# Kernel tuning notes

Measured on AMD Instinct MI355X. Metric: run time of the kernel, lower is better.

Reference implementation:

```python
import jax, jax.numpy as jnp
import numpy as np
import math

H = 1024      # d_model
NHALF = 32    # d_state // 2
B = 4
L = 4096
DT_MIN, DT_MAX = 1e-3, 1e-1


def setup_inputs() -> dict:
    key = jax.random.key(0)
    k_x, k_dt, k_c, k_d = jax.random.split(key, 4)
    x = jax.random.normal(k_x, (B, L, H), dtype=jnp.float32)
    # log-uniform dt in [dt_min, dt_max]
    log_dt = (jax.random.uniform(k_dt, (H,), dtype=jnp.float32)
              * (math.log(DT_MAX) - math.log(DT_MIN)) + math.log(DT_MIN))
    log_A_real = jnp.log(0.5 * jnp.ones((H, NHALF), dtype=jnp.float32))
    A_imag = math.pi * jnp.broadcast_to(jnp.arange(NHALF, dtype=jnp.float32), (H, NHALF))
    C = jax.random.normal(k_c, (H, NHALF, 2), dtype=jnp.float32) / math.sqrt(NHALF)
    D = jax.random.normal(k_d, (H,), dtype=jnp.float32)
    return {"x": x, "log_dt": log_dt, "log_A_real": log_A_real,
            "A_imag": A_imag, "C": C, "D": D}


def _kernel(log_dt, log_A_real, A_imag, C, L_len):
    """SSM convolution kernel, shape [H, L]."""
    dt = jnp.exp(log_dt)                                   # [H]
    A = -jnp.exp(log_A_real) + 1j * A_imag                 # [H, N/2] complex
    Cc = C[..., 0] + 1j * C[..., 1]                        # [H, N/2]
    dtA = A * dt[:, None]                                  # [H, N/2]
    Cw = Cc * (jnp.exp(dtA) - 1.0) / A                     # [H, N/2]
    l = jnp.arange(L_len)                                  # [L]
    vand = jnp.exp(dtA[..., None] * l)                     # [H, N/2, L] complex
    K = 2.0 * jnp.einsum('hn,hnl->hl', Cw, vand).real      # [H, L]
    return K


def reference(x, log_dt, log_A_real, A_imag, C, D):
    # transposed=False: x is [B, L, H] -> work in [B, H, L]
    xt = jnp.swapaxes(x, -1, -2)                           # [B, H, L]
    Lc = xt.shape[-1]
    K = _kernel(log_dt, log_A_real, A_imag, C, Lc)         # [H, L]
    n = 2 * Lc
    Kf = jnp.fft.rfft(K.astype(jnp.float32), n=n)          # [H, n//2+1]
    xf = jnp.fft.rfft(xt.astype(jnp.float32), n=n)         # [B, H, n//2+1]
    y = jnp.fft.irfft(xf * Kf, n=n)[..., :Lc]              # [B, H, L]
    y = y + xt * D[:, None]
    return jnp.swapaxes(y, -1, -2).astype(x.dtype)         # [B, L, H]
```

## Files before the change

kernel.cpp:

```cpp
#include <hip/hip_runtime.h>
#include <math.h>

#define Lc 4096
#define Hc 1024
#define Bc 4
#define NNc 32

typedef __attribute__((ext_vector_type(8))) short s8v;
typedef __attribute__((ext_vector_type(4))) float f4v;

#define SWB(r, e) ((((r) << 6) + (e)) ^ (((r) & 7) << 3))

__device__ inline unsigned short bf16_rne(float x) {
    unsigned u = __float_as_uint(x);
    unsigned r = (u + 0x7FFFu + ((u >> 16) & 1u)) >> 16;
    return (unsigned short)r;
}

__global__ __launch_bounds__(256) void split_transpose(const float* __restrict__ src,
                                                       unsigned short* __restrict__ dst) {
    __shared__ float tile[64][65];
    int b  = blockIdx.z;
    int h0 = blockIdx.x * 64;
    int l0 = blockIdx.y * 64;
    const float* s = src + (size_t)b * Lc * Hc;
    int tid = threadIdx.x;
#pragma unroll
    for (int it = 0; it < 4; it++) {
        int idx = tid + 256 * it;
        int r = idx >> 4, c4 = idx & 15;
        float4 v = *(const float4*)(s + (size_t)(l0 + r) * Hc + (h0 + 4 * c4));
        tile[r][4 * c4 + 0] = v.x;
        tile[r][4 * c4 + 1] = v.y;
        tile[r][4 * c4 + 2] = v.z;
        tile[r][4 * c4 + 3] = v.w;
    }
    __syncthreads();
#pragma unroll
    for (int it = 0; it < 8; it++) {
        int hh = it * 8 + (tid >> 5);
        int p  = tid & 31;
        float v0 = tile[2 * p + 0][hh];
        float v1 = tile[2 * p + 1][hh];
        unsigned hi = (unsigned)bf16_rne(v0) | ((unsigned)bf16_rne(v1) << 16);
        unsigned short* base = dst + (size_t)(b * Hc + h0 + hh) * 4096;
        *(unsigned*)(base + (l0 + 2 * p)) = hi;
    }
}

__global__ __launch_bounds__(256) void untranspose_bf16(const unsigned short* __restrict__ src,
                                                        float* __restrict__ dst) {
    __shared__ float tile[64][65];
    int b  = blockIdx.z;
    int h0 = blockIdx.x * 64;
    int l0 = blockIdx.y * 64;
    const unsigned short* s = src + (size_t)b * Hc * Lc;
    float* d = dst + (size_t)b * Lc * Hc;
    int tid = threadIdx.x;
#pragma unroll
    for (int it = 0; it < 8; it++) {
        int idx = tid + 256 * it;
        int hh = idx >> 5, dp = idx & 31;
        unsigned v = *(const unsigned*)(s + (size_t)(h0 + hh) * Lc + (l0 + 2 * dp));
        tile[hh][2 * dp]     = __uint_as_float((v & 0xffffu) << 16);
        tile[hh][2 * dp + 1] = __uint_as_float((v >> 16) << 16);
    }
    __syncthreads();
#pragma unroll
    for (int it = 0; it < 4; it++) {
        int idx = tid + 256 * it;
        int r = idx >> 4, c4 = idx & 15;
        f4v v;
        v.x = tile[4 * c4 + 0][r];
        v.y = tile[4 * c4 + 1][r];
        v.z = tile[4 * c4 + 2][r];
        v.w = tile[4 * c4 + 3][r];
        __builtin_nontemporal_store(v, (f4v*)(d + (size_t)(l0 + r) * Hc + (h0 + 4 * c4)));
    }
}

#define MFMA(a, b, c) __builtin_amdgcn_mfma_f32_16x16x32_bf16((a), (b), (c), 0, 0, 0)

__global__ __launch_bounds__(256, 4) void s4d_mfma9(
    const unsigned short* __restrict__ xpl,
    unsigned short* __restrict__ ypl,
    const float* __restrict__ log_dt,
    const float* __restrict__ log_A_real,
    const float* __restrict__ A_imag,
    const float* __restrict__ Cmat,
    const float* __restrict__ Dvec)
{
    __shared__ __align__(16) unsigned short WtH[4096];
    __shared__ __align__(16) unsigned short WpH[4096];
    __shared__ __align__(16) unsigned short TtH[4096];
    __shared__ __align__(16) unsigned short Elds[64 * 72];
    __shared__ float WV[256];
    __shared__ float Ktap[64];
    __shared__ float cAr[NNc], cAi[NNc], c2R[NNc], c2I[NNc], cWSr[NNc], cWSi[NNc];

    const int tid = threadIdx.x;
    const int h   = blockIdx.x;
    const int w   = tid >> 6;
    const int l   = tid & 63;
    const int l15 = l & 15;
    const int grp = l >> 4;
    const int rowoff = (16 * w + l15) * 64;

    s8v xh0, xh1;
    {
        const unsigned short* xb = xpl + (size_t)h * 4096;
        xh0 = *(const s8v*)(xb + rowoff + 8 * grp);
        xh1 = *(const s8v*)(xb + rowoff + 32 + 8 * grp);
    }

    if (tid < NNc) {
        int n = tid;
        float dtv = expf(log_dt[h]);
        float Ar = -expf(log_A_real[h * NNc + n]);
        float Ai = A_imag[h * NNc + n];
        float ar = Ar * dtv, ai = Ai * dtv;
        cAr[n] = ar; cAi[n] = ai;
        float er = expf(ar), sn, cs;
        sincosf(ai, &sn, &cs);
        float numr = er * cs - 1.f, numi = er * sn;
        float inv = 1.f / (Ar * Ar + Ai * Ai);
        float fr = (numr * Ar + numi * Ai) * inv;
        float fi = (numi * Ar - numr * Ai) * inv;
        float Ccr = Cmat[(h * NNc + n) * 2 + 0];
        float Cci = Cmat[(h * NNc + n) * 2 + 1];
        c2R[n] = 2.f * (Ccr * fr - Cci * fi);
        c2I[n] = 2.f * (Ccr * fi + Cci * fr);
        float e64 = expf(64.f * ar), s64, c64;
        sincosf(64.f * ai, &s64, &c64);
        cWSr[n] = e64 * c64; cWSi[n] = e64 * s64;
    }
    __syncthreads();

    {
        int p = tid >> 2, q = tid & 3;
        float acc = 0.f;
#pragma unroll
        for (int i = 0; i < 8; i++) {
            int n = 8 * q + i;
            float fp = (float)p;
            float e = __expf(cAr[n] * fp);
            float sn = __sinf(cAi[n] * fp), cs = __cosf(cAi[n] * fp);
            acc += e * (c2R[n] * cs - c2I[n] * sn);
        }
        WV[p * 4 + q] = acc;
    }
#pragma unroll
    for (int m = 0; m < 2; m++) {
        int u = tid + 256 * m;
        int r = u >> 3, jc = u & 7;
        {
            int n = r & 31, im = r >> 5;
            s8v hv;
#pragma unroll
            for (int i = 0; i < 8; i++) {
                float p = (float)(63 - (jc * 8 + i));
                float e = __expf(cAr[n] * p);
                float sn = __sinf(cAi[n] * p), cs = __cosf(cAi[n] * p);
                hv[i] = (short)bf16_rne(e * (im ? sn : cs));
            }
            *(s8v*)&WtH[SWB(r, jc * 8)] = hv;
        }
        {
            float p = (float)(r + 1);
            s8v hv;
#pragma unroll
            for (int i = 0; i < 8; i++) {
                int c = jc * 8 + i;
                int n = c >> 1;
                float e = __expf(cAr[n] * p);
                float sn = __sinf(cAi[n] * p), cs = __cosf(cAi[n] * p);
                hv[i] = (short)bf16_rne(e * ((c & 1) ? -sn : cs));
            }
            *(s8v*)&WpH[SWB(r, jc * 8)] = hv;
        }
    }
    __syncthreads();

    if (tid < 64) {
        float k = WV[tid * 4] + WV[tid * 4 + 1] + WV[tid * 4 + 2] + WV[tid * 4 + 3];
        if (tid == 0) k += Dvec[h];
        Ktap[tid] = k;
    }
    __syncthreads();

#pragma unroll
    for (int m = 0; m < 2; m++) {
        int u = tid + 256 * m;
        int r = u >> 3, jc = u & 7;
        s8v hv;
#pragma unroll
        for (int i = 0; i < 8; i++) {
            int j = jc * 8 + i;
            hv[i] = (short)bf16_rne((j <= r) ? Ktap[r - j] : 0.f);
        }
        *(s8v*)&TtH[SWB(r, jc * 8)] = hv;
    }

    float qR[2], qI[2], q4R[2], q4I[2], qgR[2], qgI[2], q16R[2], q16I[2], cwR[2], cwI[2];
#pragma unroll
    for (int md = 0; md < 2; md++) {
        int n = md * 16 + l15;
        float qr = cWSr[n], qi = cWSi[n];
        float q2r = fmaf(qr, qr, -(qi * qi)),    q2i = 2.f * qr * qi;
        float q4r = fmaf(q2r, q2r, -(q2i * q2i)), q4i = 2.f * q2r * q2i;
        float q8r = fmaf(q4r, q4r, -(q4i * q4i)), q8i = 2.f * q4r * q4i;
        float q16r = fmaf(q8r, q8r, -(q8i * q8i)), q16i = 2.f * q8r * q8i;
        float q12r = fmaf(q8r, q4r, -(q8i * q4i)), q12i = fmaf(q8r, q4i, q8i * q4r);
        qR[md] = qr; qI[md] = qi;
        q4R[md] = q4r; q4I[md] = q4i;
        qgR[md] = (grp == 0) ? 1.f : (grp == 1) ? q4r : (grp == 2) ? q8r : q12r;
        qgI[md] = (grp == 0) ? 0.f : (grp == 1) ? q4i : (grp == 2) ? q8i : q12i;
        q16R[md] = q16r; q16I[md] = q16i;
        cwR[md] = c2R[n]; cwI[md] = c2I[n];
    }
    __syncthreads();

#pragma unroll
    for (int b = 0; b < Bc; b++) {
        s8v nh0, nh1;
        if (b < Bc - 1) {
            const unsigned short* xb = xpl + (size_t)((b + 1) * Hc + h) * 4096;
            nh0 = *(const s8v*)(xb + rowoff + 8 * grp);
            nh1 = *(const s8v*)(xb + rowoff + 32 + 8 * grp);
        }

        f4v acc[4];
#pragma unroll
        for (int tj = 0; tj < 4; tj++) {
            int row = tj * 16 + l15;
            s8v bh0 = *(const s8v*)&WtH[SWB(row, 8 * grp)];
            s8v bh1 = *(const s8v*)&WtH[SWB(row, 32 + 8 * grp)];
            f4v a = {0.f, 0.f, 0.f, 0.f};
            a = MFMA(xh0, bh0, a);
            a = MFMA(xh1, bh1, a);
            acc[tj] = a;
        }

        float exr[2][4], exi[2][4], gcr[2], gci[2];
#pragma unroll
        for (int md = 0; md < 2; md++) {
            float qr = qR[md], qi = qI[md];
            float e1r = acc[md][0],                       e1i = acc[md + 2][0];
            float e2r = fmaf(qr, e1r, fmaf(-qi, e1i, acc[md][1]));
            float e2i = fmaf(qr, e1i, fmaf( qi, e1r, acc[md + 2][1]));
            float e3r = fmaf(qr, e2r, fmaf(-qi, e2i, acc[md][2]));
            float e3i = fmaf(qr, e2i, fmaf( qi, e2r, acc[md + 2][2]));
            float tr  = fmaf(qr, e3r, fmaf(-qi, e3i, acc[md][3]));
            float ti  = fmaf(qr, e3i, fmaf( qi, e3r, acc[md + 2][3]));
            exr[md][0] = 0.f; exi[md][0] = 0.f;
            exr[md][1] = e1r; exi[md][1] = e1i;
            exr[md][2] = e2r; exi[md][2] = e2i;
            exr[md][3] = e3r; exi[md][3] = e3i;
            float t1r = __shfl_up(tr, 16u, 64), t1i = __shfl_up(ti, 16u, 64);
            float t2r = __shfl_up(tr, 32u, 64), t2i = __shfl_up(ti, 32u, 64);
            float t3r = __shfl_up(tr, 48u, 64), t3i = __shfl_up(ti, 48u, 64);
            if (grp < 1) { t1r = 0.f; t1i = 0.f; }
            if (grp < 2) { t2r = 0.f; t2i = 0.f; }
            if (grp < 3) { t3r = 0.f; t3i = 0.f; }
            float q4r = q4R[md], q4i = q4I[md];
            float q8r = fmaf(q4r, q4r, -(q4i * q4i)), q8i = 2.f * q4r * q4i;
            float gr = t1r, gi = t1i;
            gr = fmaf(q4r, t2r, fmaf(-q4i, t2i, gr));
            gi = fmaf(q4r, t2i, fmaf( q4i, t2r, gi));
            gr = fmaf(q8r, t3r, fmaf(-q8i, t3i, gr));
            gi = fmaf(q8r, t3i, fmaf( q8i, t3r, gi));
            gcr[md] = gr; gci[md] = gi;
            float wvr = fmaf(q4r, gr, fmaf(-q4i, gi, tr));
            float wvi = fmaf(q4r, gi, fmaf( q4i, gr, ti));
            if (l >= 48) {
                int n = md * 16 + l15;
                WV[w * 64 + 2 * n]     = wvr;
                WV[w * 64 + 2 * n + 1] = wvi;
            }
        }
        __syncthreads();

#pragma unroll
        for (int md = 0; md < 2; md++) {
            int n = md * 16 + l15;
            float wcr = 0.f, wci = 0.f;
            if (w >= 1) {
                wcr = WV[(w - 1) * 64 + 2 * n];
                wci = WV[(w - 1) * 64 + 2 * n + 1];
            }
            if (w >= 2) {
                float vr = WV[(w - 2) * 64 + 2 * n], vi = WV[(w - 2) * 64 + 2 * n + 1];
                wcr = fmaf(q16R[md], vr, fmaf(-q16I[md], vi, wcr));
                wci = fmaf(q16R[md], vi, fmaf( q16I[md], vr, wci));
            }
            if (w >= 3) {
                float q32r = fmaf(q16R[md], q16R[md], -(q16I[md] * q16I[md]));
                float q32i = 2.f * q16R[md] * q16I[md];
                float vr = WV[(w - 3) * 64 + 2 * n], vi = WV[(w - 3) * 64 + 2 * n + 1];
                wcr = fmaf(q32r, vr, fmaf(-q32i, vi, wcr));
                wci = fmaf(q32r, vi, fmaf( q32i, vr, wci));
            }
            float cir = fmaf(qgR[md], wcr, fmaf(-qgI[md], wci, gcr[md]));
            float cii = fmaf(qgR[md], wci, fmaf( qgI[md], wcr, gci[md]));
            float qr = qR[md], qi = qI[md];
            float q2r = fmaf(qr, qr, -(qi * qi)),  q2i = 2.f * qr * qi;
            float q3r = fmaf(q2r, qr, -(q2i * qi)), q3i = fmaf(q2r, qi, q2i * qr);
            float pr[4] = {1.f, qr, q2r, q3r};
            float pi[4] = {0.f, qi, q2i, q3i};
#pragma unroll
            for (int r2 = 0; r2 < 4; r2++) {
                float Gr2 = fmaf(pr[r2], cir, fmaf(-pi[r2], cii, exr[md][r2]));
                float Gi2 = fmaf(pr[r2], cii, fmaf( pi[r2], cir, exi[md][r2]));
                float Er2 = fmaf(cwR[md], Gr2, -(cwI[md] * Gi2));
                float Ei2 = fmaf(cwR[md], Gi2,  (cwI[md] * Gr2));
                unsigned pk = (unsigned)bf16_rne(Er2) | ((unsigned)bf16_rne(Ei2) << 16);
                int chunk = 16 * w + 4 * grp + r2;
                *(unsigned*)&Elds[chunk * 72 + 2 * n] = pk;
            }
        }
        __syncthreads();

        s8v ee0 = *(const s8v*)&Elds[(16 * w + l15) * 72 + 8 * grp];
        s8v ee1 = *(const s8v*)&Elds[(16 * w + l15) * 72 + 32 + 8 * grp];
        unsigned short* yp = ypl + (size_t)(b * Hc + h) * 4096;
#pragma unroll
        for (int tj = 0; tj < 4; tj++) {
            int row = tj * 16 + l15;
            int i0 = SWB(row, 8 * grp);
            int i1 = SWB(row, 32 + 8 * grp);
            s8v th0 = *(const s8v*)&TtH[i0];
            s8v th1 = *(const s8v*)&TtH[i1];
            s8v ph0 = *(const s8v*)&WpH[i0];
            s8v ph1 = *(const s8v*)&WpH[i1];
            f4v a = {0.f, 0.f, 0.f, 0.f};
            a = MFMA(xh0, th0, a);
            a = MFMA(xh1, th1, a);
            a = MFMA(ee0, ph0, a);
            a = MFMA(ee1, ph1, a);
#pragma unroll
            for (int r2 = 0; r2 < 4; r2++) {
                int chunk = 16 * w + 4 * grp + r2;
                yp[chunk * 64 + row] = bf16_rne(a[r2]);
            }
        }

        if (b < Bc - 1) { xh0 = nh0; xh1 = nh1; }
    }
}

extern "C" void kernel_launch(void* const* d_in, const int* in_sizes, int n_in,
                              void* d_out, int out_size, void* d_ws, size_t ws_size,
                              hipStream_t stream) {
    const float* x          = (const float*)d_in[0];
    const float* log_dt     = (const float*)d_in[1];
    const float* log_A_real = (const float*)d_in[2];
    const float* A_imag     = (const float*)d_in[3];
    const float* Cmat       = (const float*)d_in[4];
    const float* Dvec       = (const float*)d_in[5];
    float* out = (float*)d_out;

    const size_t plane = (size_t)Bc * Hc * Lc;
    const size_t need  = plane * sizeof(unsigned short);
    if (ws_size < need) return;

    unsigned short* xpl = (unsigned short*)d_ws;

    split_transpose<<<dim3(Hc / 64, Lc / 64, Bc), 256, 0, stream>>>(x, xpl);
    s4d_mfma9<<<Hc, 256, 0, stream>>>(xpl, xpl, log_dt, log_A_real, A_imag, Cmat, Dvec);
    untranspose_bf16<<<dim3(Hc / 64, Lc / 64, Bc), 256, 0, stream>>>(xpl, out);
}
```

Baseline: 62.44 us.

## Hold Toeplitz tap fragments in registers, swap MFMA operands, pack output stores

The per-channel Toeplitz tap matrix is now built directly into register fragments instead of an LDS tile, which removes the TtH buffer and its reads inside the batch loop. The output MFMAs take their operands in swapped order, so each lane's four accumulator values are contiguous along L and go out as one packed 8-byte store instead of four scattered 2-byte stores. WV is double-buffered by batch parity, and the barrier after the Elds writes is dropped because each wave only reads back the chunks it wrote itself. Powers of q are recomputed on the fly instead of being held across the loop, trading extra ALU work and the register-held tap fragments for lower register pressure elsewhere.

```diff
diff --git a/kernel.cpp b/kernel.cpp
--- a/kernel.cpp
+++ b/kernel.cpp
@@ -8,6 +8,7 @@
 
 typedef __attribute__((ext_vector_type(8))) short s8v;
 typedef __attribute__((ext_vector_type(4))) float f4v;
+typedef __attribute__((ext_vector_type(2))) unsigned int u2v;
 
 #define SWB(r, e) ((((r) << 6) + (e)) ^ (((r) & 7) << 3))
 
@@ -81,7 +82,7 @@
 
 #define MFMA(a, b, c) __builtin_amdgcn_mfma_f32_16x16x32_bf16((a), (b), (c), 0, 0, 0)
 
-__global__ __launch_bounds__(256, 4) void s4d_mfma9(
+__global__ __launch_bounds__(256, 4) void s4d_mfma10(
     const unsigned short* __restrict__ xpl,
     unsigned short* __restrict__ ypl,
     const float* __restrict__ log_dt,
@@ -92,9 +93,8 @@
 {
     __shared__ __align__(16) unsigned short WtH[4096];
     __shared__ __align__(16) unsigned short WpH[4096];
-    __shared__ __align__(16) unsigned short TtH[4096];
     __shared__ __align__(16) unsigned short Elds[64 * 72];
-    __shared__ float WV[256];
+    __shared__ float WV[512];
     __shared__ float Ktap[64];
     __shared__ float cAr[NNc], cAi[NNc], c2R[NNc], c2I[NNc], cWSr[NNc], cWSi[NNc];
 
@@ -188,34 +188,34 @@
     }
     __syncthreads();
 
-#pragma unroll
-    for (int m = 0; m < 2; m++) {
-        int u = tid + 256 * m;
-        int r = u >> 3, jc = u & 7;
-        s8v hv;
-#pragma unroll
-        for (int i = 0; i < 8; i++) {
-            int j = jc * 8 + i;
-            hv[i] = (short)bf16_rne((j <= r) ? Ktap[r - j] : 0.f);
-        }
-        *(s8v*)&TtH[SWB(r, jc * 8)] = hv;
-    }
-
-    float qR[2], qI[2], q4R[2], q4I[2], qgR[2], qgI[2], q16R[2], q16I[2], cwR[2], cwI[2];
+    s8v tf[4][2];
+#pragma unroll
+    for (int tj = 0; tj < 4; tj++) {
+        int row = tj * 16 + l15;
+#pragma unroll
+        for (int hf = 0; hf < 2; hf++) {
+            int kb = 32 * hf + 8 * grp;
+            s8v v;
+#pragma unroll
+            for (int i = 0; i < 8; i++) {
+                int idx = row - kb - i;
+                int ic = idx < 0 ? 0 : idx;
+                float kv = Ktap[ic];
+                v[i] = (short)bf16_rne(idx < 0 ? 0.f : kv);
+            }
+            tf[tj][hf] = v;
+        }
+    }
+
+    float qR[2], qI[2], q4R[2], q4I[2], cwR[2], cwI[2];
 #pragma unroll
     for (int md = 0; md < 2; md++) {
         int n = md * 16 + l15;
         float qr = cWSr[n], qi = cWSi[n];
-        float q2r = fmaf(qr, qr, -(qi * qi)),    q2i = 2.f * qr * qi;
-        float q4r = fmaf(q2r, q2r, -(q2i * q2i)), q4i = 2.f * q2r * q2i;
-        float q8r = fmaf(q4r, q4r, -(q4i * q4i)), q8i = 2.f * q4r * q4i;
-        float q16r = fmaf(q8r, q8r, -(q8i * q8i)), q16i = 2.f * q8r * q8i;
-        float q12r = fmaf(q8r, q4r, -(q8i * q4i)), q12i = fmaf(q8r, q4i, q8i * q4r);
+        float q2r = fmaf(qr, qr, -(qi * qi)),     q2i = 2.f * qr * qi;
         qR[md] = qr; qI[md] = qi;
-        q4R[md] = q4r; q4I[md] = q4i;
-        qgR[md] = (grp == 0) ? 1.f : (grp == 1) ? q4r : (grp == 2) ? q8r : q12r;
-        qgI[md] = (grp == 0) ? 0.f : (grp == 1) ? q4i : (grp == 2) ? q8i : q12i;
-        q16R[md] = q16r; q16I[md] = q16i;
+        q4R[md] = fmaf(q2r, q2r, -(q2i * q2i));
+        q4I[md] = 2.f * q2r * q2i;
         cwR[md] = c2R[n]; cwI[md] = c2I[n];
     }
     __syncthreads();
@@ -228,6 +228,7 @@
             nh0 = *(const s8v*)(xb + rowoff + 8 * grp);
             nh1 = *(const s8v*)(xb + rowoff + 32 + 8 * grp);
         }
+        float* wv = &WV[(b & 1) * 256];
 
         f4v acc[4];
 #pragma unroll
@@ -274,8 +275,8 @@
             float wvi = fmaf(q4r, gi, fmaf( q4i, gr, ti));
             if (l >= 48) {
                 int n = md * 16 + l15;
-                WV[w * 64 + 2 * n]     = wvr;
-                WV[w * 64 + 2 * n + 1] = wvi;
+                wv[w * 64 + 2 * n]     = wvr;
+                wv[w * 64 + 2 * n + 1] = wvi;
             }
         }
         __syncthreads();
@@ -283,27 +284,33 @@
 #pragma unroll
         for (int md = 0; md < 2; md++) {
             int n = md * 16 + l15;
+            float q4r = q4R[md], q4i = q4I[md];
+            float q8r = fmaf(q4r, q4r, -(q4i * q4i)),  q8i = 2.f * q4r * q4i;
+            float q12r = fmaf(q8r, q4r, -(q8i * q4i)), q12i = fmaf(q8r, q4i, q8i * q4r);
+            float q16r = fmaf(q8r, q8r, -(q8i * q8i)), q16i = 2.f * q8r * q8i;
             float wcr = 0.f, wci = 0.f;
             if (w >= 1) {
-                wcr = WV[(w - 1) * 64 + 2 * n];
-                wci = WV[(w - 1) * 64 + 2 * n + 1];
+                wcr = wv[(w - 1) * 64 + 2 * n];
+                wci = wv[(w - 1) * 64 + 2 * n + 1];
             }
             if (w >= 2) {
-                float vr = WV[(w - 2) * 64 + 2 * n], vi = WV[(w - 2) * 64 + 2 * n + 1];
-                wcr = fmaf(q16R[md], vr, fmaf(-q16I[md], vi, wcr));
-                wci = fmaf(q16R[md], vi, fmaf( q16I[md], vr, wci));
+                float vr = wv[(w - 2) * 64 + 2 * n], vi = wv[(w - 2) * 64 + 2 * n + 1];
+                wcr = fmaf(q16r, vr, fmaf(-q16i, vi, wcr));
+                wci = fmaf(q16r, vi, fmaf( q16i, vr, wci));
             }
             if (w >= 3) {
-                float q32r = fmaf(q16R[md], q16R[md], -(q16I[md] * q16I[md]));
-                float q32i = 2.f * q16R[md] * q16I[md];
-                float vr = WV[(w - 3) * 64 + 2 * n], vi = WV[(w - 3) * 64 + 2 * n + 1];
+                float q32r = fmaf(q16r, q16r, -(q16i * q16i));
+                float q32i = 2.f * q16r * q16i;
+                float vr = wv[(w - 3) * 64 + 2 * n], vi = wv[(w - 3) * 64 + 2 * n + 1];
                 wcr = fmaf(q32r, vr, fmaf(-q32i, vi, wcr));
                 wci = fmaf(q32r, vi, fmaf( q32i, vr, wci));
             }
-            float cir = fmaf(qgR[md], wcr, fmaf(-qgI[md], wci, gcr[md]));
-            float cii = fmaf(qgR[md], wci, fmaf( qgI[md], wcr, gci[md]));
+            float qgr = (grp == 0) ? 1.f : (grp == 1) ? q4r : (grp == 2) ? q8r : q12r;
+            float qgi = (grp == 0) ? 0.f : (grp == 1) ? q4i : (grp == 2) ? q8i : q12i;
+            float cir = fmaf(qgr, wcr, fmaf(-qgi, wci, gcr[md]));
+            float cii = fmaf(qgr, wci, fmaf( qgi, wcr, gci[md]));
             float qr = qR[md], qi = qI[md];
-            float q2r = fmaf(qr, qr, -(qi * qi)),  q2i = 2.f * qr * qi;
+            float q2r = fmaf(qr, qr, -(qi * qi)),   q2i = 2.f * qr * qi;
             float q3r = fmaf(q2r, qr, -(q2i * qi)), q3i = fmaf(q2r, qi, q2i * qr);
             float pr[4] = {1.f, qr, q2r, q3r};
             float pi[4] = {0.f, qi, q2i, q3i};
@@ -318,7 +325,6 @@
                 *(unsigned*)&Elds[chunk * 72 + 2 * n] = pk;
             }
         }
-        __syncthreads();
 
         s8v ee0 = *(const s8v*)&Elds[(16 * w + l15) * 72 + 8 * grp];
         s8v ee1 = *(const s8v*)&Elds[(16 * w + l15) * 72 + 32 + 8 * grp];
@@ -326,22 +332,17 @@
 #pragma unroll
         for (int tj = 0; tj < 4; tj++) {
             int row = tj * 16 + l15;
-            int i0 = SWB(row, 8 * grp);
-            int i1 = SWB(row, 32 + 8 * grp);
-            s8v th0 = *(const s8v*)&TtH[i0];
-            s8v th1 = *(const s8v*)&TtH[i1];
-            s8v ph0 = *(const s8v*)&WpH[i0];
-            s8v ph1 = *(const s8v*)&WpH[i1];
+            s8v ph0 = *(const s8v*)&WpH[SWB(row, 8 * grp)];
+            s8v ph1 = *(const s8v*)&WpH[SWB(row, 32 + 8 * grp)];
             f4v a = {0.f, 0.f, 0.f, 0.f};
-            a = MFMA(xh0, th0, a);
-            a = MFMA(xh1, th1, a);
-            a = MFMA(ee0, ph0, a);
-            a = MFMA(ee1, ph1, a);
-#pragma unroll
-            for (int r2 = 0; r2 < 4; r2++) {
-                int chunk = 16 * w + 4 * grp + r2;
-                yp[chunk * 64 + row] = bf16_rne(a[r2]);
-            }
+            a = MFMA(tf[tj][0], xh0, a);
+            a = MFMA(tf[tj][1], xh1, a);
+            a = MFMA(ph0, ee0, a);
+            a = MFMA(ph1, ee1, a);
+            u2v pk;
+            pk.x = (unsigned)bf16_rne(a[0]) | ((unsigned)bf16_rne(a[1]) << 16);
+            pk.y = (unsigned)bf16_rne(a[2]) | ((unsigned)bf16_rne(a[3]) << 16);
+            *(u2v*)(yp + (16 * w + l15) * 64 + tj * 16 + 4 * grp) = pk;
         }
 
         if (b < Bc - 1) { xh0 = nh0; xh1 = nh1; }
@@ -366,6 +367,6 @@
     unsigned short* xpl = (unsigned short*)d_ws;
 
     split_transpose<<<dim3(Hc / 64, Lc / 64, Bc), 256, 0, stream>>>(x, xpl);
-    s4d_mfma9<<<Hc, 256, 0, stream>>>(xpl, xpl, log_dt, log_A_real, A_imag, Cmat, Dvec);
+    s4d_mfma10<<<Hc, 256, 0, stream>>>(xpl, xpl, log_dt, log_A_real, A_imag, Cmat, Dvec);
     untranspose_bf16<<<dim3(Hc / 64, Lc / 64, Bc), 256, 0, stream>>>(xpl, out);
 }
```

Result: slower. 99.98 us (+60.1%).
